# Performance work log

Hardware: AMD Instinct MI355X
Metric: run time of the kernel (lower is better)

## Reference

```python
import jax, jax.numpy as jnp
import numpy as np

K_PER_CLASS = 10
WINDOW = 7
MIN_MASS = 0.05
EPS = 1e-8


def _pool_sum(x, w):
    # sum-pool over last two dims, stride 1, zero padding w//2 (count_include_pad avg = sum / w^2)
    nd = x.ndim
    return jax.lax.reduce_window(
        x, 0.0, jax.lax.add,
        (1,) * (nd - 2) + (w, w),
        (1,) * nd,
        [(0, 0)] * (nd - 2) + [(w // 2, w // 2)] * 2,
    )


def _l2norm(x, axis):
    # matches torch F.normalize(p=2): x / max(||x||, 1e-12)
    return x / jnp.maximum(jnp.linalg.norm(x, axis=axis, keepdims=True), 1e-12)


def setup_inputs() -> dict:
    key = jax.random.key(0)
    k1, k2, k3 = jax.random.split(key, 3)
    feature_map = jax.random.normal(k1, (8, 512, 96, 96), dtype=jnp.float32)
    prototypes = jax.random.normal(k2, (80, 512), dtype=jnp.float32)
    pseudo_mask = jax.random.randint(k3, (8, 96, 96), 0, 9, dtype=jnp.int32)
    return {"feature_map": feature_map, "prototypes": prototypes, "pseudo_mask": pseudo_mask}


def reference(feature_map, prototypes, pseudo_mask):
    B, D, H, W = feature_map.shape
    K = K_PER_CLASS
    C = prototypes.shape[0] // K
    area = WINDOW * WINDOW

    Fn = _l2norm(feature_map, 1)                       # [B,D,H,W]
    Pn = _l2norm(prototypes, 1).reshape(C, K, D)       # [C,K,D]
    sim = jnp.einsum('bdhw,ckd->bckhw', Fn, Pn)        # [B,C,K,H,W]

    omega = (pseudo_mask[:, None] == (jnp.arange(C) + 1)[None, :, None, None]).astype(sim.dtype)  # [B,C,H,W]

    num = _pool_sum(sim * omega[:, :, None], WINDOW) / area   # [B,C,K,H,W]
    den = _pool_sum(omega, WINDOW) / area                      # [B,C,H,W]
    region = num / (den[:, :, None] + EPS)

    a = region.reshape(B, C, K, H * W).transpose(0, 1, 3, 2)   # [B,C,HW,K]
    valid = (den > MIN_MASS).reshape(B, C, H * W)
    V = valid.sum(-1)                                          # [B,C] int
    Vf = jnp.maximum(V, 1).astype(a.dtype)
    vm = valid[..., None].astype(a.dtype)

    mean = (a * vm).sum(2) / Vf[..., None]                     # [B,C,K]
    a_c = (a - mean[:, :, None]) * vm                          # zero out invalid rows
    nrm = jnp.sqrt((a_c * a_c).sum(2))                         # [B,C,K]
    a_n = a_c / (nrm[:, :, None] + EPS)

    gram = jnp.einsum('bcvk,bcvl->bckl', a_n, a_n) / Vf[..., None, None]  # [B,C,K,K]
    off = gram * (1.0 - jnp.eye(K, dtype=gram.dtype))
    loss_c = (off * off).sum((-1, -2)) / (K * (K - 1))         # [B,C]

    active = (omega.sum((-1, -2)) >= 1.0) & (V >= 2)           # mirrors skip conditions
    af = active.astype(loss_c.dtype)
    per_image = (loss_c * af).sum(-1) / jnp.maximum(af.sum(-1), 1.0)
    return per_image.sum() / B
```

## Files before the change

kernel.cpp:

```cpp
#include <hip/hip_runtime.h>
#include <cstdint>
#include <cstddef>

namespace {
constexpr int Bn = 8, Dn = 512, Hn = 96, Wn = 96, HWn = Hn * Wn;
constexpr int Cn = 8, Kn = 10, CKn = Cn * Kn;
constexpr int NPIX = Bn * HWn;
constexpr int NMOM = 66;
constexpr int RSTRIP = 8;
constexpr float EPSF = 1e-8f;
constexpr float MINM = 0.05f;

constexpr size_t oPnT = 0;
constexpr size_t oS   = oPnT + (size_t)Dn * CKn;
constexpr size_t oMom = oS + (size_t)Bn * Kn * HWn;
constexpr size_t oCnt = oMom + 64 * NMOM;
constexpr size_t oEnd = oCnt + 64;
}

__device__ __forceinline__ float wred64(float v) {
#pragma unroll
    for (int o = 32; o > 0; o >>= 1) v += __shfl_down(v, o, 64);
    return v;
}

__global__ __launch_bounds__(64) void k_protonorm(const float* __restrict__ P,
                                                  float* __restrict__ PnT) {
    int ck = blockIdx.x, lane = threadIdx.x;
    float v[8]; float ss = 0.f;
#pragma unroll
    for (int j = 0; j < 8; ++j) { v[j] = P[ck * Dn + lane + 64 * j]; ss += v[j] * v[j]; }
    ss = wred64(ss);
    ss = __shfl(ss, 0, 64);
    float inv = 1.0f / fmaxf(sqrtf(ss), 1e-12f);
#pragma unroll
    for (int j = 0; j < 8; ++j)
        PnT[(size_t)(lane + 64 * j) * CKn + ck] = v[j] * inv;
}

__global__ __launch_bounds__(256) void k_sim(const float* __restrict__ F,
                                             const float* __restrict__ PnT,
                                             const int* __restrict__ mask,
                                             float* __restrict__ S,
                                             int* __restrict__ cnt) {
    __shared__ float pch[64 * 96];
    __shared__ int hist[Cn];
    const int tid = threadIdx.x;
    const int pixLocal = tid & 63;
    const int g = tid >> 6;
    const int pix = blockIdx.x * 64 + pixLocal;
    const int b = pix / HWn, hw = pix % HWn;
    if (tid < Cn) hist[tid] = 0;

    const int m = mask[pix];
    const int cc = m > 0 ? m - 1 : 0;

    float acc[Kn]; float ss = 0.f;
#pragma unroll
    for (int k = 0; k < Kn; ++k) acc[k] = 0.f;

    for (int p = 0; p < 8; ++p) {
        __syncthreads();
        for (int i = tid; i < 64 * CKn; i += 256) {
            int sd = i / CKn, ck = i % CKn;
            int sg = sd >> 4, dd = sd & 15;
            int gd = sg * 128 + p * 16 + dd;
            int c = ck / Kn, kk = ck % Kn;
            pch[sd * 96 + c * 12 + kk] = PnT[(size_t)gd * CKn + ck];
        }
        __syncthreads();
        const float* Fp = &F[(size_t)(b * Dn + g * 128 + p * 16) * HWn + hw];
#pragma unroll
        for (int dd = 0; dd < 16; ++dd) {
            float f = Fp[(size_t)dd * HWn];
            ss += f * f;
            const float4* p4 = (const float4*)&pch[(g * 16 + dd) * 96 + cc * 12];
            float4 pa = p4[0], pb = p4[1];
            float2 pc = *(const float2*)&pch[(g * 16 + dd) * 96 + cc * 12 + 8];
            acc[0] += f * pa.x; acc[1] += f * pa.y; acc[2] += f * pa.z; acc[3] += f * pa.w;
            acc[4] += f * pb.x; acc[5] += f * pb.y; acc[6] += f * pb.z; acc[7] += f * pb.w;
            acc[8] += f * pc.x; acc[9] += f * pc.y;
        }
    }
    __syncthreads();
    float* red = pch;
#pragma unroll
    for (int k = 0; k < Kn; ++k) red[g * 768 + pixLocal * 12 + k] = acc[k];
    red[g * 768 + pixLocal * 12 + 10] = ss;
    __syncthreads();
    if (tid < 64) {
        float tot[11];
#pragma unroll
        for (int j = 0; j < 11; ++j)
            tot[j] = red[tid * 12 + j] + red[768 + tid * 12 + j] +
                     red[1536 + tid * 12 + j] + red[2304 + tid * 12 + j];
        float inv = 1.0f / fmaxf(sqrtf(tot[10]), 1e-12f);
#pragma unroll
        for (int k = 0; k < Kn; ++k)
            S[(size_t)(b * Kn + k) * HWn + hw] = tot[k] * inv;
        if (m > 0) atomicAdd(&hist[m - 1], 1);
    }
    __syncthreads();
    if (tid < Cn) atomicAdd(&cnt[((blockIdx.x * 64) / HWn) * Cn + tid], hist[tid]);
}

__global__ __launch_bounds__(256) void k_pool(const int* __restrict__ mask,
                                              const float* __restrict__ S,
                                              float* __restrict__ mom) {
    __shared__ float sNum[Kn][14 * 96];
    __shared__ float sDen[14 * 96];
    __shared__ float red[4][NMOM];
    const int bc = blockIdx.x / 12, strip = blockIdx.x % 12;
    const int c = bc & 7, b = bc >> 3;
    const int h0 = strip * RSTRIP;
    const int tid = threadIdx.x;

    for (int item = tid; item < 14 * 24; item += 256) {
        const int r = item / 24, wg = item % 24;
        const int hh = h0 - 3 + r;
        const int w0 = wg * 4;
        float a[Kn][4];
        float dn[4] = {0.f, 0.f, 0.f, 0.f};
#pragma unroll
        for (int k = 0; k < Kn; ++k)
#pragma unroll
            for (int o = 0; o < 4; ++o) a[k][o] = 0.f;

        if (hh >= 0 && hh < Hn) {
            const int rowb = b * HWn + hh * Wn;
            const float* Srow = &S[(size_t)b * Kn * HWn + hh * Wn];
#pragma unroll
            for (int dc = -3; dc <= 6; ++dc) {
                int ww = w0 + dc;
                if (ww < 0 || ww >= Wn) continue;
                const int olo = dc - 3 > 0 ? dc - 3 : 0;
                const int ohi = dc + 3 < 3 ? dc + 3 : 3;
                if (mask[rowb + ww] == c + 1) {
#pragma unroll
                    for (int o = 0; o < 4; ++o)
                        if (o >= olo && o <= ohi) dn[o] += 1.0f;
#pragma unroll
                    for (int k = 0; k < Kn; ++k) {
                        float s = Srow[(size_t)k * HWn + ww];
#pragma unroll
                        for (int o = 0; o < 4; ++o)
                            if (o >= olo && o <= ohi) a[k][o] += s;
                    }
                }
            }
        }
#pragma unroll
        for (int o = 0; o < 4; ++o) {
            sDen[r * 96 + w0 + o] = dn[o];
#pragma unroll
            for (int k = 0; k < Kn; ++k) sNum[k][r * 96 + w0 + o] = a[k][o];
        }
    }
    __syncthreads();

    float mm[NMOM];
#pragma unroll
    for (int i = 0; i < NMOM; ++i) mm[i] = 0.f;

    for (int out = tid; out < RSTRIP * 96; out += 256) {
        const int oh = out / 96, w = out % 96;
        float den = 0.f;
        float n[Kn];
#pragma unroll
        for (int k = 0; k < Kn; ++k) n[k] = 0.f;
#pragma unroll
        for (int dr = 0; dr < 7; ++dr) {
            const int r = oh + dr;
            den += sDen[r * 96 + w];
#pragma unroll
            for (int k = 0; k < Kn; ++k) n[k] += sNum[k][r * 96 + w];
        }
        float dA = den * (1.0f / 49.0f);
        float inv = 1.0f / (dA + EPSF);
        float vm = (dA > MINM) ? 1.0f : 0.0f;
        float rr[Kn];
#pragma unroll
        for (int k = 0; k < Kn; ++k)
            rr[k] = n[k] * (1.0f / 49.0f) * inv * vm;
        mm[0] += vm;
#pragma unroll
        for (int k = 0; k < Kn; ++k) mm[1 + k] += rr[k];
        int p = 11;
#pragma unroll
        for (int k = 0; k < Kn; ++k)
#pragma unroll
            for (int l = 0; l <= k; ++l, ++p) mm[p] += rr[k] * rr[l];
    }

    const int lane = tid & 63, wv = tid >> 6;
#pragma unroll
    for (int i = 0; i < NMOM; ++i) {
        float x = wred64(mm[i]);
        if (lane == 0) red[wv][i] = x;
    }
    __syncthreads();
    for (int i = tid; i < NMOM; i += 256)
        atomicAdd(&mom[bc * NMOM + i],
                  red[0][i] + red[1][i] + red[2][i] + red[3][i]);
}

__global__ __launch_bounds__(64) void k_final(const float* __restrict__ mom,
                                              const int* __restrict__ cnt,
                                              float* __restrict__ out) {
    const int bc = threadIdx.x;
    float mo[NMOM];
#pragma unroll
    for (int i = 0; i < NMOM; ++i) mo[i] = mom[bc * NMOM + i];
    const float V = mo[0];
    const float Vf = fmaxf(V, 1.0f);
    float Sk[Kn];
#pragma unroll
    for (int k = 0; k < Kn; ++k) Sk[k] = mo[1 + k];

    float M[55];
    {
        int p = 0;
#pragma unroll
        for (int k = 0; k < Kn; ++k)
#pragma unroll
            for (int l = 0; l <= k; ++l, ++p)
                M[p] = mo[11 + p] - Sk[k] * Sk[l] / Vf;
    }
    float nrm[Kn];
#pragma unroll
    for (int k = 0; k < Kn; ++k)
        nrm[k] = sqrtf(fmaxf(M[k * (k + 1) / 2 + k], 0.0f));
    float loss = 0.f;
    {
        int p = 0;
#pragma unroll
        for (int k = 0; k < Kn; ++k) {
#pragma unroll
            for (int l = 0; l <= k; ++l, ++p) {
                if (l == k) continue;
                float g = M[p] / ((nrm[k] + EPSF) * (nrm[l] + EPSF)) / Vf;
                loss += 2.0f * g * g;
            }
        }
    }
    loss *= 1.0f / (float)(Kn * (Kn - 1));
    bool act = (cnt[bc] >= 1) && (V >= 2.0f);
    float sl = act ? loss : 0.f;
    float sa = act ? 1.f : 0.f;
#pragma unroll
    for (int o = 4; o > 0; o >>= 1) {
        sl += __shfl_down(sl, o, 8);
        sa += __shfl_down(sa, o, 8);
    }
    __shared__ float pimg[Bn];
    if ((bc & 7) == 0) pimg[bc >> 3] = sl / fmaxf(sa, 1.0f);
    __syncthreads();
    if (bc == 0) {
        float tot = 0.f;
#pragma unroll
        for (int b = 0; b < Bn; ++b) tot += pimg[b];
        out[0] = tot / (float)Bn;
    }
}

extern "C" void kernel_launch(void* const* d_in, const int* in_sizes, int n_in,
                              void* d_out, int out_size, void* d_ws, size_t ws_size,
                              hipStream_t stream) {
    const float* F  = (const float*)d_in[0];
    const float* P  = (const float*)d_in[1];
    const int* mask = (const int*)d_in[2];
    float* ws = (float*)d_ws;
    float* out = (float*)d_out;

    hipMemsetAsync(ws + oMom, 0, (oEnd - oMom) * sizeof(float), stream);

    k_protonorm<<<CKn, 64, 0, stream>>>(P, ws + oPnT);
    k_sim<<<NPIX / 64, 256, 0, stream>>>(F, ws + oPnT, mask, ws + oS,
                                         (int*)(ws + oCnt));
    k_pool<<<64 * 12, 256, 0, stream>>>(mask, ws + oS, ws + oMom);
    k_final<<<1, 64, 0, stream>>>(ws + oMom, (const int*)(ws + oCnt), out);
}
```

Before: 319.8 us.

## Split sim reduction over D-chunks across grid with separate reduce kernel

The similarity kernel now gives each thread a full pixel and splits the 512-channel reduction across a second grid dimension of four chunks. Partial dot products and sums of squares go to a global workspace, and a new kernel sums them, normalises, and builds the class histogram. Prototypes are pre-laid out in padded per-class rows, so the shared-memory fill becomes a straight float4 copy with no index math. This removes the in-block shared reduction and the scattered prototype staging. In exchange it adds about 11 floats of partial traffic per pixel per chunk and an extra kernel launch.

```diff
diff --git a/kernel.cpp b/kernel.cpp
--- a/kernel.cpp
+++ b/kernel.cpp
@@ -6,16 +6,19 @@
 constexpr int Bn = 8, Dn = 512, Hn = 96, Wn = 96, HWn = Hn * Wn;
 constexpr int Cn = 8, Kn = 10, CKn = Cn * Kn;
 constexpr int NPIX = Bn * HWn;
+constexpr int NCHUNK = 4, DCH = Dn / NCHUNK;
 constexpr int NMOM = 66;
 constexpr int RSTRIP = 8;
+constexpr int PROW = 96;
 constexpr float EPSF = 1e-8f;
 constexpr float MINM = 0.05f;
 
-constexpr size_t oPnT = 0;
-constexpr size_t oS   = oPnT + (size_t)Dn * CKn;
-constexpr size_t oMom = oS + (size_t)Bn * Kn * HWn;
-constexpr size_t oCnt = oMom + 64 * NMOM;
-constexpr size_t oEnd = oCnt + 64;
+constexpr size_t oPnTp = 0;
+constexpr size_t oS    = oPnTp + (size_t)Dn * PROW;
+constexpr size_t oPart = oS + (size_t)Bn * Kn * HWn;
+constexpr size_t oMom  = oPart + (size_t)NCHUNK * 11 * NPIX;
+constexpr size_t oCnt  = oMom + 64 * NMOM;
+constexpr size_t oEnd  = oCnt + 64;
 }
 
 __device__ __forceinline__ float wred64(float v) {
@@ -25,8 +28,9 @@
 }
 
 __global__ __launch_bounds__(64) void k_protonorm(const float* __restrict__ P,
-                                                  float* __restrict__ PnT) {
+                                                  float* __restrict__ PnTp) {
     int ck = blockIdx.x, lane = threadIdx.x;
+    const int c = ck / Kn, kk = ck % Kn;
     float v[8]; float ss = 0.f;
 #pragma unroll
     for (int j = 0; j < 8; ++j) { v[j] = P[ck * Dn + lane + 64 * j]; ss += v[j] * v[j]; }
@@ -35,22 +39,18 @@
     float inv = 1.0f / fmaxf(sqrtf(ss), 1e-12f);
 #pragma unroll
     for (int j = 0; j < 8; ++j)
-        PnT[(size_t)(lane + 64 * j) * CKn + ck] = v[j] * inv;
+        PnTp[(size_t)(lane + 64 * j) * PROW + c * 12 + kk] = v[j] * inv;
 }
 
 __global__ __launch_bounds__(256) void k_sim(const float* __restrict__ F,
-                                             const float* __restrict__ PnT,
-                                             const int* __restrict__ mask,
-                                             float* __restrict__ S,
-                                             int* __restrict__ cnt) {
-    __shared__ float pch[64 * 96];
-    __shared__ int hist[Cn];
+                                             const float* __restrict__ PnTp,
+                                             float* __restrict__ part,
+                                             const int* __restrict__ mask) {
+    __shared__ float pch[64 * PROW];
     const int tid = threadIdx.x;
-    const int pixLocal = tid & 63;
-    const int g = tid >> 6;
-    const int pix = blockIdx.x * 64 + pixLocal;
+    const int pix = blockIdx.x * 256 + tid;
+    const int chunk = blockIdx.y;
     const int b = pix / HWn, hw = pix % HWn;
-    if (tid < Cn) hist[tid] = 0;
 
     const int m = mask[pix];
     const int cc = m > 0 ? m - 1 : 0;
@@ -59,49 +59,65 @@
 #pragma unroll
     for (int k = 0; k < Kn; ++k) acc[k] = 0.f;
 
-    for (int p = 0; p < 8; ++p) {
+    for (int p = 0; p < DCH / 64; ++p) {
+        const int dbase = chunk * DCH + p * 64;
         __syncthreads();
-        for (int i = tid; i < 64 * CKn; i += 256) {
-            int sd = i / CKn, ck = i % CKn;
-            int sg = sd >> 4, dd = sd & 15;
-            int gd = sg * 128 + p * 16 + dd;
-            int c = ck / Kn, kk = ck % Kn;
-            pch[sd * 96 + c * 12 + kk] = PnT[(size_t)gd * CKn + ck];
+        {
+            const float4* src = (const float4*)&PnTp[(size_t)dbase * PROW];
+            float4* dst = (float4*)pch;
+#pragma unroll
+            for (int i = 0; i < 6; ++i)
+                dst[tid + 256 * i] = src[tid + 256 * i];
         }
         __syncthreads();
-        const float* Fp = &F[(size_t)(b * Dn + g * 128 + p * 16) * HWn + hw];
-#pragma unroll
-        for (int dd = 0; dd < 16; ++dd) {
-            float f = Fp[(size_t)dd * HWn];
+#pragma unroll 4
+        for (int dd = 0; dd < 64; ++dd) {
+            float f = F[(size_t)(b * Dn + dbase + dd) * HWn + hw];
             ss += f * f;
-            const float4* p4 = (const float4*)&pch[(g * 16 + dd) * 96 + cc * 12];
+            const float4* p4 = (const float4*)&pch[dd * PROW + cc * 12];
             float4 pa = p4[0], pb = p4[1];
-            float2 pc = *(const float2*)&pch[(g * 16 + dd) * 96 + cc * 12 + 8];
+            float2 pc = *(const float2*)&pch[dd * PROW + cc * 12 + 8];
             acc[0] += f * pa.x; acc[1] += f * pa.y; acc[2] += f * pa.z; acc[3] += f * pa.w;
             acc[4] += f * pb.x; acc[5] += f * pb.y; acc[6] += f * pb.z; acc[7] += f * pb.w;
             acc[8] += f * pc.x; acc[9] += f * pc.y;
         }
     }
-    __syncthreads();
-    float* red = pch;
-#pragma unroll
-    for (int k = 0; k < Kn; ++k) red[g * 768 + pixLocal * 12 + k] = acc[k];
-    red[g * 768 + pixLocal * 12 + 10] = ss;
-    __syncthreads();
-    if (tid < 64) {
-        float tot[11];
-#pragma unroll
-        for (int j = 0; j < 11; ++j)
-            tot[j] = red[tid * 12 + j] + red[768 + tid * 12 + j] +
-                     red[1536 + tid * 12 + j] + red[2304 + tid * 12 + j];
-        float inv = 1.0f / fmaxf(sqrtf(tot[10]), 1e-12f);
-#pragma unroll
-        for (int k = 0; k < Kn; ++k)
-            S[(size_t)(b * Kn + k) * HWn + hw] = tot[k] * inv;
-        if (m > 0) atomicAdd(&hist[m - 1], 1);
-    }
-    __syncthreads();
-    if (tid < Cn) atomicAdd(&cnt[((blockIdx.x * 64) / HWn) * Cn + tid], hist[tid]);
+#pragma unroll
+    for (int k = 0; k < Kn; ++k)
+        part[(size_t)(chunk * 11 + k) * NPIX + pix] = acc[k];
+    part[(size_t)(chunk * 11 + 10) * NPIX + pix] = ss;
+}
+
+__global__ __launch_bounds__(256) void k_simred(const float* __restrict__ part,
+                                                const int* __restrict__ mask,
+                                                float* __restrict__ S,
+                                                int* __restrict__ cnt) {
+    __shared__ int hist[Cn];
+    const int tid = threadIdx.x;
+    const int pix = blockIdx.x * 256 + tid;
+    if (tid < Cn) hist[tid] = 0;
+    __syncthreads();
+
+    float acc[Kn]; float ss = 0.f;
+#pragma unroll
+    for (int k = 0; k < Kn; ++k) acc[k] = 0.f;
+#pragma unroll
+    for (int ch = 0; ch < NCHUNK; ++ch) {
+#pragma unroll
+        for (int k = 0; k < Kn; ++k)
+            acc[k] += part[(size_t)(ch * 11 + k) * NPIX + pix];
+        ss += part[(size_t)(ch * 11 + 10) * NPIX + pix];
+    }
+    float inv = 1.0f / fmaxf(sqrtf(ss), 1e-12f);
+    const int b = pix / HWn, hw = pix % HWn;
+#pragma unroll
+    for (int k = 0; k < Kn; ++k)
+        S[(size_t)(b * Kn + k) * HWn + hw] = acc[k] * inv;
+
+    const int m = mask[pix];
+    if (m > 0) atomicAdd(&hist[m - 1], 1);
+    __syncthreads();
+    if (tid < Cn) atomicAdd(&cnt[(pix / HWn) * Cn + tid], hist[tid]);
 }
 
 __global__ __launch_bounds__(256) void k_pool(const int* __restrict__ mask,
@@ -274,9 +290,11 @@
 
     hipMemsetAsync(ws + oMom, 0, (oEnd - oMom) * sizeof(float), stream);
 
-    k_protonorm<<<CKn, 64, 0, stream>>>(P, ws + oPnT);
-    k_sim<<<NPIX / 64, 256, 0, stream>>>(F, ws + oPnT, mask, ws + oS,
-                                         (int*)(ws + oCnt));
+    k_protonorm<<<CKn, 64, 0, stream>>>(P, ws + oPnTp);
+    k_sim<<<dim3(NPIX / 256, NCHUNK), 256, 0, stream>>>(F, ws + oPnTp,
+                                                        ws + oPart, mask);
+    k_simred<<<NPIX / 256, 256, 0, stream>>>(ws + oPart, mask, ws + oS,
+                                             (int*)(ws + oCnt));
     k_pool<<<64 * 12, 256, 0, stream>>>(mask, ws + oS, ws + oMom);
     k_final<<<1, 64, 0, stream>>>(ws + oMom, (const int*)(ws + oCnt), out);
 }
```

Measured after the change: 287.0 us. -10.3%, faster.
